# Performance work log

Measured on AMD Instinct MI355X. Metric: run time of the kernel, lower is better.

## Reference

```python
import jax, jax.numpy as jnp
import numpy as np

N = 100000
K = 27  # 3^3 kernel offsets for dimension=3
EPS = 1e-6


def layer_norm(x, gamma, beta):
    mu = jnp.mean(x, axis=-1, keepdims=True)
    var = jnp.mean(jnp.square(x - mu), axis=-1, keepdims=True)
    return (x - mu) * jax.lax.rsqrt(var + EPS) * gamma + beta


def sparse_conv3(x, idx, mask, W):
    # gather-GEMM-scatter form of Minkowski sparse conv:
    # x: [N, Cin], idx/mask: [N, K], W: [K, Cin, Cout]
    xg = jnp.where(mask[..., None], x[idx], 0.0)  # [N, K, Cin]
    return jnp.einsum('nkc,kcd->nd', xg, W)


def setup_inputs() -> dict:
    key = jax.random.key(0)
    ks = jax.random.split(key, 6)
    x = jax.random.normal(ks[0], (N, 32), dtype=jnp.float32)
    neighbor_idx = jax.random.randint(ks[1], (N, K), 0, N, dtype=jnp.int32)
    neighbor_mask = jax.random.randint(ks[2], (N, K), 0, 2) > 0
    W_conv = jax.random.normal(ks[3], (32, 32), dtype=jnp.float32) * 0.1
    W1 = jax.random.normal(ks[4], (K, 32, 128), dtype=jnp.float32) * 0.05
    W2 = jax.random.normal(ks[5], (K, 128, 32), dtype=jnp.float32) * 0.05
    return {
        'x': x,
        'neighbor_idx': neighbor_idx,
        'neighbor_mask': neighbor_mask,
        'W_conv': W_conv,
        'gamma0': jnp.ones((32,), jnp.float32),
        'beta0': jnp.zeros((32,), jnp.float32),
        'W1': W1,
        'gamma1': jnp.ones((128,), jnp.float32),
        'beta1': jnp.zeros((128,), jnp.float32),
        'W2': W2,
        'gamma2': jnp.ones((32,), jnp.float32),
        'beta2': jnp.zeros((32,), jnp.float32),
    }


def reference(x, neighbor_idx, neighbor_mask, W_conv, gamma0, beta0,
              W1, gamma1, beta1, W2, gamma2, beta2):
    gelu = lambda t: jax.nn.gelu(t, approximate=False)  # torch default (erf)
    residual = x
    out = x @ W_conv                      # kernel_size=1 conv == dense matmul
    out = gelu(layer_norm(out, gamma0, beta0))
    out = sparse_conv3(out, neighbor_idx, neighbor_mask, W1)
    out = gelu(layer_norm(out, gamma1, beta1))
    out = sparse_conv3(out, neighbor_idx, neighbor_mask, W2)
    out = layer_norm(out, gamma2, beta2)
    out = out + residual
    return gelu(out)
```

## Files before the change

kernel.cpp:

```cpp
#include <hip/hip_runtime.h>
#include <hip/hip_bf16.h>
#include <math.h>

#define NPTS 100000
#define KOFF 27

typedef __attribute__((ext_vector_type(8))) __bf16 bf16x8;
typedef __attribute__((ext_vector_type(4))) float f32x4;

__device__ __forceinline__ unsigned short f2bf(float f) {
    unsigned int u = __float_as_uint(f);
    u += 0x7fffu + ((u >> 16) & 1u);
    return (unsigned short)(u >> 16);
}

__device__ __forceinline__ float gelu_erf(float v) {
    return 0.5f * v * (1.0f + erff(v * 0.70710678118654752f));
}

__global__ __launch_bounds__(256)
void repack_kernel(const float* __restrict__ W1, const float* __restrict__ W2,
                   const void* __restrict__ maskp,
                   unsigned short* __restrict__ W1p,
                   unsigned short* __restrict__ W2p,
                   unsigned short* __restrict__ W2q,
                   int* __restrict__ flagp) {
    int o = blockIdx.x * 256 + threadIdx.x;
    if (o == 0) {
        const unsigned int* mw = (const unsigned int*)maskp;
        int f = 0;
        for (int i = 0; i < 64; ++i) f |= (mw[i] > 1u) ? 1 : 0;
        *flagp = f;
    }
    if (o < KOFF * 32 * 128) {
        int j = o & 7, lane = (o >> 3) & 63;
        int quad = lane >> 4, nn = lane & 15;
        int ct1 = (o >> 9) & 7, k1 = o >> 12;
        int kk1 = quad * 8 + j;
        W1p[o] = f2bf(W1[(k1 * 32 + kk1) * 128 + (ct1 * 16 + nn)]);
        int ct2 = (o >> 9) & 1, kc2 = (o >> 10) & 3, k2 = o >> 12;
        int kk2 = kc2 * 32 + quad * 8 + j;
        W2p[o] = f2bf(W2[(k2 * 128 + kk2) * 32 + (ct2 * 16 + nn)]);
        W2q[o] = f2bf(W2[(k2 * 128 + kk2) * 32 + (2 * nn + ct2)]);
    }
}

__global__ __launch_bounds__(256)
void conv1_ln_gelu(const float* __restrict__ x, const float* __restrict__ Wc,
                   const float* __restrict__ g0, const float* __restrict__ b0,
                   unsigned short* __restrict__ out0) {
    __shared__ float xs[256];
    __shared__ float wc[1024];
    int t = threadIdx.x;
    int nb = blockIdx.x * 8;
    xs[t] = x[nb * 32 + t];
    for (int i = t; i < 1024; i += 256) wc[i] = Wc[i];
    __syncthreads();
    int r = t >> 5, d = t & 31;
    const float* xr = &xs[r * 32];
    float v = 0.f;
#pragma unroll
    for (int c = 0; c < 32; ++c) v = fmaf(xr[c], wc[c * 32 + d], v);
    float s = v, s2 = v * v;
#pragma unroll
    for (int m = 16; m >= 1; m >>= 1) {
        s  += __shfl_xor(s,  m, 32);
        s2 += __shfl_xor(s2, m, 32);
    }
    float mu  = s * (1.f / 32.f);
    float var = s2 * (1.f / 32.f) - mu * mu;
    float y = (v - mu) * rsqrtf(var + 1e-6f) * g0[d] + b0[d];
    out0[nb * 32 + t] = f2bf(gelu_erf(y));
}

__device__ __forceinline__ void stage_gidx64(int* s_gidx, const int* nidx,
                                             const void* maskp, int mflag,
                                             int nb, int t) {
    int cnt = (NPTS - nb < 64 ? NPTS - nb : 64) * KOFF;
    for (int i = t; i < 64 * KOFF; i += 64) {
        int g = -1;
        if (i < cnt) {
            int gi = nidx[nb * KOFF + i];
            int m = mflag ? (int)((const unsigned char*)maskp)[nb * KOFF + i]
                          : ((const int*)maskp)[nb * KOFF + i];
            g = m ? gi : -1;
        }
        s_gidx[i] = g;
    }
}

__global__ __launch_bounds__(64, 2)
void conv_k1(const int* __restrict__ nidx, const void* __restrict__ maskp,
             const int* __restrict__ flagp,
             const unsigned short* __restrict__ out0,
             const unsigned short* __restrict__ W1p,
             const float* __restrict__ g1, const float* __restrict__ b1,
             unsigned short* __restrict__ out1) {
    __shared__ int s_gidx[32 * KOFF];

    int t = threadIdx.x;
    int nb = blockIdx.x * 32;
    int mflag = *flagp;
    {
        for (int i = t; i < 32 * KOFF; i += 64) {
            int gi = nidx[nb * KOFF + i];
            int m = mflag ? (int)((const unsigned char*)maskp)[nb * KOFF + i]
                          : ((const int*)maskp)[nb * KOFF + i];
            s_gidx[i] = m ? gi : -1;
        }
    }
    __syncthreads();

    int lane = t & 63;
    int mrow = lane & 15, quad = lane >> 4;
    const unsigned short* a_base = out0 + quad * 8;
    const int* gp0 = &s_gidx[(0 * 16 + mrow) * KOFF];
    const int* gp1 = &s_gidx[(1 * 16 + mrow) * KOFF];

    f32x4 acc[2][8] = {};
    bf16x8 a[3][2], b[3][8];

#pragma unroll
    for (int d = 0; d < 2; ++d) {
        const unsigned short* wb = W1p + (((d * 8) * 64 + lane) << 3);
#pragma unroll
        for (int ct = 0; ct < 8; ++ct)
            b[d][ct] = *reinterpret_cast<const bf16x8*>(wb + ((ct * 64) << 3));
        int g0 = gp0[d], g1i = gp1[d];
        a[d][0] = bf16x8{}; if (g0  >= 0) a[d][0] = *reinterpret_cast<const bf16x8*>(a_base + g0  * 32);
        a[d][1] = bf16x8{}; if (g1i >= 0) a[d][1] = *reinterpret_cast<const bf16x8*>(a_base + g1i * 32);
    }

#pragma unroll
    for (int k = 0; k < KOFF; ++k) {
        if (k + 2 < KOFF) {
            int s = (k + 2) % 3;
            const unsigned short* wb = W1p + ((((k + 2) * 8) * 64 + lane) << 3);
#pragma unroll
            for (int ct = 0; ct < 8; ++ct)
                b[s][ct] = *reinterpret_cast<const bf16x8*>(wb + ((ct * 64) << 3));
            int g0 = gp0[k + 2], g1i = gp1[k + 2];
            a[s][0] = bf16x8{}; if (g0  >= 0) a[s][0] = *reinterpret_cast<const bf16x8*>(a_base + g0  * 32);
            a[s][1] = bf16x8{}; if (g1i >= 0) a[s][1] = *reinterpret_cast<const bf16x8*>(a_base + g1i * 32);
        }
#pragma unroll
        for (int rt = 0; rt < 2; ++rt)
#pragma unroll
            for (int ct = 0; ct < 8; ++ct)
                acc[rt][ct] = __builtin_amdgcn_mfma_f32_16x16x32_bf16(a[k % 3][rt], b[k % 3][ct], acc[rt][ct], 0, 0, 0);
    }

    float gv[8], bv[8];
#pragma unroll
    for (int ct = 0; ct < 8; ++ct) {
        gv[ct] = g1[ct * 16 + mrow];
        bv[ct] = b1[ct * 16 + mrow];
    }
#pragma unroll
    for (int rt = 0; rt < 2; ++rt) {
        int n_base = nb + rt * 16 + quad * 4;
#pragma unroll
        for (int r = 0; r < 4; ++r) {
            float s = 0.f, s2 = 0.f;
#pragma unroll
            for (int ct = 0; ct < 8; ++ct) { float v = acc[rt][ct][r]; s += v; s2 += v * v; }
#pragma unroll
            for (int m = 1; m <= 8; m <<= 1) {
                s  += __shfl_xor(s,  m, 16);
                s2 += __shfl_xor(s2, m, 16);
            }
            float mu = s * (1.f / 128.f);
            float rs = rsqrtf(s2 * (1.f / 128.f) - mu * mu + 1e-6f);
            int n = n_base + r;
#pragma unroll
            for (int ct = 0; ct < 8; ++ct) {
                float y = (acc[rt][ct][r] - mu) * rs * gv[ct] + bv[ct];
                out1[n * 128 + ct * 16 + mrow] = f2bf(gelu_erf(y));
            }
        }
    }
}

__global__ __launch_bounds__(64, 2)
void gemm_tmp(const unsigned short* __restrict__ out1,
              const unsigned short* __restrict__ W2q,
              unsigned short* __restrict__ tmp) {
    int t = threadIdx.x;
    int nb = blockIdx.x * 64;
    int mrow = t & 15, quad = t >> 4;

    bf16x8 a[4][4];
#pragma unroll
    for (int rt = 0; rt < 4; ++rt) {
        int n = nb + rt * 16 + mrow;
        bool ok = (n < NPTS);
#pragma unroll
        for (int kc = 0; kc < 4; ++kc) {
            a[rt][kc] = bf16x8{};
            if (ok)
                a[rt][kc] = *reinterpret_cast<const bf16x8*>(out1 + (size_t)n * 128 + kc * 32 + quad * 8);
        }
    }
    bf16x8 b[2][8];
    {
        const unsigned short* wb = W2q + (t << 3);
#pragma unroll
        for (int f = 0; f < 8; ++f)
            b[0][f] = *reinterpret_cast<const bf16x8*>(wb + ((f * 64) << 3));
    }

#pragma unroll
    for (int k = 0; k < KOFF; ++k) {
        int cur = k & 1, nxt = cur ^ 1;
        if (k + 1 < KOFF) {
            const unsigned short* wb = W2q + ((((k + 1) * 8) * 64 + t) << 3);
#pragma unroll
            for (int f = 0; f < 8; ++f)
                b[nxt][f] = *reinterpret_cast<const bf16x8*>(wb + ((f * 64) << 3));
        }
        f32x4 acc[4][2] = {};
#pragma unroll
        for (int rt = 0; rt < 4; ++rt)
#pragma unroll
            for (int kc = 0; kc < 4; ++kc) {
                acc[rt][0] = __builtin_amdgcn_mfma_f32_16x16x32_bf16(a[rt][kc], b[cur][kc * 2 + 0], acc[rt][0], 0, 0, 0);
                acc[rt][1] = __builtin_amdgcn_mfma_f32_16x16x32_bf16(a[rt][kc], b[cur][kc * 2 + 1], acc[rt][1], 0, 0, 0);
            }
        unsigned int* tk32 = (unsigned int*)(tmp + (size_t)k * NPTS * 32);
#pragma unroll
        for (int rt = 0; rt < 4; ++rt) {
            int n0 = nb + rt * 16 + quad * 4;
#pragma unroll
            for (int r = 0; r < 4; ++r) {
                int n = n0 + r;
                if (n < NPTS) {
                    unsigned int pk = (unsigned int)f2bf(acc[rt][0][r])
                                    | ((unsigned int)f2bf(acc[rt][1][r]) << 16);
                    tk32[(size_t)n * 16 + mrow] = pk;
                }
            }
        }
    }
}

__global__ __launch_bounds__(256)
void gather_sum(const int* __restrict__ nidx, const void* __restrict__ maskp,
                const int* __restrict__ flagp,
                const unsigned short* __restrict__ tmp,
                const float* __restrict__ g2, const float* __restrict__ b2,
                const float* __restrict__ x, float* __restrict__ outp) {
    __shared__ int s_gidx[64 * KOFF];
    int t = threadIdx.x;
    int nb = blockIdx.x * 64;
    int mflag = *flagp;
    int cnt = (NPTS - nb < 64 ? NPTS - nb : 64) * KOFF;
    for (int i = t; i < 64 * KOFF; i += 256) {
        int g = -1;
        if (i < cnt) {
            int gi = nidx[nb * KOFF + i];
            int m = mflag ? (int)((const unsigned char*)maskp)[nb * KOFF + i]
                          : ((const int*)maskp)[nb * KOFF + i];
            g = m ? gi : -1;
        }
        s_gidx[i] = g;
    }
    __syncthreads();

    int rl = t >> 2, q = t & 3;
    const int* gp = &s_gidx[rl * KOFF];
    const unsigned short* tq = tmp + q * 8;

    float acc[8] = {};
    uint4 ring[4];
#pragma unroll
    for (int d = 0; d < 4; ++d) {
        int g = gp[d];
        ring[d] = uint4{0u, 0u, 0u, 0u};
        if (g >= 0)
            ring[d] = *reinterpret_cast<const uint4*>(tq + ((size_t)d * NPTS + g) * 32);
    }
#pragma unroll
    for (int k = 0; k < KOFF; ++k) {
        uint4 v = ring[k & 3];
        if (k + 4 < KOFF) {
            int g = gp[k + 4];
            ring[k & 3] = uint4{0u, 0u, 0u, 0u};
            if (g >= 0)
                ring[k & 3] = *reinterpret_cast<const uint4*>(tq + ((size_t)(k + 4) * NPTS + g) * 32);
        }
        unsigned int w0 = v.x, w1 = v.y, w2 = v.z, w3 = v.w;
        acc[0] += __uint_as_float(w0 << 16);
        acc[1] += __uint_as_float(w0 & 0xffff0000u);
        acc[2] += __uint_as_float(w1 << 16);
        acc[3] += __uint_as_float(w1 & 0xffff0000u);
        acc[4] += __uint_as_float(w2 << 16);
        acc[5] += __uint_as_float(w2 & 0xffff0000u);
        acc[6] += __uint_as_float(w3 << 16);
        acc[7] += __uint_as_float(w3 & 0xffff0000u);
    }

    float s = 0.f, s2 = 0.f;
#pragma unroll
    for (int j = 0; j < 8; ++j) { s += acc[j]; s2 += acc[j] * acc[j]; }
    s += __shfl_xor(s, 1); s2 += __shfl_xor(s2, 1);
    s += __shfl_xor(s, 2); s2 += __shfl_xor(s2, 2);
    float mu = s * (1.f / 32.f);
    float rs = rsqrtf(s2 * (1.f / 32.f) - mu * mu + 1e-6f);

    int n = nb + rl;
    if (n < NPTS) {
        float o[8];
#pragma unroll
        for (int j = 0; j < 8; ++j) {
            int c = q * 8 + j;
            float y = (acc[j] - mu) * rs * g2[c] + b2[c] + x[n * 32 + c];
            o[j] = gelu_erf(y);
        }
        *reinterpret_cast<float4*>(outp + n * 32 + q * 8)     = make_float4(o[0], o[1], o[2], o[3]);
        *reinterpret_cast<float4*>(outp + n * 32 + q * 8 + 4) = make_float4(o[4], o[5], o[6], o[7]);
    }
}

__global__ __launch_bounds__(64, 2)
void conv_k2_fb(const int* __restrict__ nidx, const void* __restrict__ maskp,
                const int* __restrict__ flagp,
                const unsigned short* __restrict__ out1,
                const unsigned short* __restrict__ W2p,
                const float* __restrict__ g2, const float* __restrict__ b2,
                const float* __restrict__ x, float* __restrict__ outp) {
    __shared__ int s_gidx[64 * KOFF];

    int t = threadIdx.x;
    int nb = blockIdx.x * 64;
    int mflag = *flagp;
    stage_gidx64(s_gidx, nidx, maskp, mflag, nb, t);
    __syncthreads();

    int lane = t & 63;
    int mrow = lane & 15, quad = lane >> 4;
    const unsigned short* a_base = out1 + quad * 8;
    const int* gp0 = &s_gidx[(0 * 16 + mrow) * KOFF];
    const int* gp1 = &s_gidx[(1 * 16 + mrow) * KOFF];
    const int* gp2 = &s_gidx[(2 * 16 + mrow) * KOFF];
    const int* gp3 = &s_gidx[(3 * 16 + mrow) * KOFF];

    f32x4 acc[4][2] = {};
    bf16x8 a[2][4][4], b[2][8];

    {
        const unsigned short* wb = W2p + (lane << 3);
#pragma unroll
        for (int f = 0; f < 8; ++f)
            b[0][f] = *reinterpret_cast<const bf16x8*>(wb + ((f * 64) << 3));
        int gg[4] = { gp0[0], gp1[0], gp2[0], gp3[0] };
#pragma unroll
        for (int rt = 0; rt < 4; ++rt) {
#pragma unroll
            for (int kc = 0; kc < 4; ++kc) a[0][rt][kc] = bf16x8{};
            if (gg[rt] >= 0) {
#pragma unroll
                for (int kc = 0; kc < 4; ++kc)
                    a[0][rt][kc] = *reinterpret_cast<const bf16x8*>(a_base + (size_t)gg[rt] * 128 + kc * 32);
            }
        }
    }

#pragma unroll
    for (int k = 0; k < KOFF; ++k) {
        int cur = k & 1, nxt = cur ^ 1;
        if (k + 1 < KOFF) {
            const unsigned short* wb = W2p + ((((k + 1) * 8) * 64 + lane) << 3);
#pragma unroll
            for (int f = 0; f < 8; ++f)
                b[nxt][f] = *reinterpret_cast<const bf16x8*>(wb + ((f * 64) << 3));
            int gg[4] = { gp0[k + 1], gp1[k + 1], gp2[k + 1], gp3[k + 1] };
#pragma unroll
            for (int rt = 0; rt < 4; ++rt) {
#pragma unroll
                for (int kc = 0; kc < 4; ++kc) a[nxt][rt][kc] = bf16x8{};
                if (gg[rt] >= 0) {
#pragma unroll
                    for (int kc = 0; kc < 4; ++kc)
                        a[nxt][rt][kc] = *reinterpret_cast<const bf16x8*>(a_base + (size_t)gg[rt] * 128 + kc * 32);
                }
            }
        }
#pragma unroll
        for (int rt = 0; rt < 4; ++rt)
#pragma unroll
            for (int kc = 0; kc < 4; ++kc) {
                acc[rt][0] = __builtin_amdgcn_mfma_f32_16x16x32_bf16(a[cur][rt][kc], b[cur][kc * 2 + 0], acc[rt][0], 0, 0, 0);
                acc[rt][1] = __builtin_amdgcn_mfma_f32_16x16x32_bf16(a[cur][rt][kc], b[cur][kc * 2 + 1], acc[rt][1], 0, 0, 0);
            }
    }

    float gv0 = g2[mrow], gv1 = g2[mrow + 16];
    float bv0 = b2[mrow], bv1 = b2[mrow + 16];
#pragma unroll
    for (int rt = 0; rt < 4; ++rt) {
        int n_base = nb + rt * 16 + quad * 4;
#pragma unroll
        for (int r = 0; r < 4; ++r) {
            float v0 = acc[rt][0][r], v1 = acc[rt][1][r];
            float s = v0 + v1, s2 = v0 * v0 + v1 * v1;
#pragma unroll
            for (int m = 1; m <= 8; m <<= 1) {
                s  += __shfl_xor(s,  m, 16);
                s2 += __shfl_xor(s2, m, 16);
            }
            float mu = s * (1.f / 32.f);
            float rs = rsqrtf(s2 * (1.f / 32.f) - mu * mu + 1e-6f);
            int n = n_base + r;
            if (n < NPTS) {
                float y0 = (v0 - mu) * rs * gv0 + bv0 + x[n * 32 + mrow];
                float y1 = (v1 - mu) * rs * gv1 + bv1 + x[n * 32 + mrow + 16];
                outp[n * 32 + mrow]      = gelu_erf(y0);
                outp[n * 32 + mrow + 16] = gelu_erf(y1);
            }
        }
    }
}

extern "C" void kernel_launch(void* const* d_in, const int* in_sizes, int n_in,
                              void* d_out, int out_size, void* d_ws, size_t ws_size,
                              hipStream_t stream) {
    const float* x    = (const float*)d_in[0];
    const int*   nidx = (const int*)d_in[1];
    const void*  maskp = d_in[2];
    const float* Wc = (const float*)d_in[3];
    const float* g0 = (const float*)d_in[4];
    const float* b0 = (const float*)d_in[5];
    const float* W1 = (const float*)d_in[6];
    const float* g1 = (const float*)d_in[7];
    const float* b1 = (const float*)d_in[8];
    const float* W2 = (const float*)d_in[9];
    const float* g2 = (const float*)d_in[10];
    const float* b2 = (const float*)d_in[11];

    char* ws = (char*)d_ws;
    unsigned short* out0 = (unsigned short*)ws;
    unsigned short* out1 = (unsigned short*)(ws + 6400000);
    unsigned short* W1p  = (unsigned short*)(ws + 32000000);
    unsigned short* W2p  = (unsigned short*)(ws + 32221184);
    unsigned short* W2q  = (unsigned short*)(ws + 32442368);
    int* flagp           = (int*)(ws + 32663552);
    unsigned short* tmp  = (unsigned short*)(ws + 32663616);
    const size_t NEED_TMP = 32663616UL + (size_t)KOFF * NPTS * 32 * 2;

    repack_kernel<<<432, 256, 0, stream>>>(W1, W2, maskp, W1p, W2p, W2q, flagp);
    conv1_ln_gelu<<<NPTS / 8, 256, 0, stream>>>(x, Wc, g0, b0, out0);
    conv_k1<<<NPTS / 32, 64, 0, stream>>>(nidx, maskp, flagp, out0, W1p, g1, b1, out1);
    if (ws_size >= NEED_TMP) {
        gemm_tmp<<<(NPTS + 63) / 64, 64, 0, stream>>>(out1, W2q, tmp);
        gather_sum<<<(NPTS + 63) / 64, 256, 0, stream>>>(nidx, maskp, flagp, tmp, g2, b2, x, (float*)d_out);
    } else {
        conv_k2_fb<<<(NPTS + 63) / 64, 64, 0, stream>>>(nidx, maskp, flagp, out1, W2p, g2, b2, x, (float*)d_out);
    }
}
```

Before: 269.7 us.

## Share W1 slices through LDS across four waves in first sparse conv

The first sparse-conv kernel now runs 256-thread blocks covering 128 points. Four waves share W1 weight slices staged in LDS, six kernel offsets per phase, instead of each 64-thread block reading the weights from global memory itself. Gather prefetch depth grows from 2 to 4 offsets. This cuts redundant global and L2 weight traffic, but adds block-wide barriers between phases, more registers and a larger LDS footprint, which may reduce occupancy.

New measurement: 287.3 us. +6.5%, slower.

```diff
diff --git a/kernel.cpp b/kernel.cpp
--- a/kernel.cpp
+++ b/kernel.cpp
@@ -89,65 +89,100 @@
     }
 }
 
-__global__ __launch_bounds__(64, 2)
+#define RPB 128
+#define PH_SL 6
+
+__global__ __launch_bounds__(256, 2)
 void conv_k1(const int* __restrict__ nidx, const void* __restrict__ maskp,
              const int* __restrict__ flagp,
              const unsigned short* __restrict__ out0,
              const unsigned short* __restrict__ W1p,
              const float* __restrict__ g1, const float* __restrict__ b1,
              unsigned short* __restrict__ out1) {
-    __shared__ int s_gidx[32 * KOFF];
+    __shared__ int s_gidx[RPB * KOFF];
+    __shared__ unsigned short b_lds[PH_SL * 4096];
 
     int t = threadIdx.x;
-    int nb = blockIdx.x * 32;
+    int nb = blockIdx.x * RPB;
     int mflag = *flagp;
+
     {
-        for (int i = t; i < 32 * KOFF; i += 64) {
-            int gi = nidx[nb * KOFF + i];
-            int m = mflag ? (int)((const unsigned char*)maskp)[nb * KOFF + i]
-                          : ((const int*)maskp)[nb * KOFF + i];
-            s_gidx[i] = m ? gi : -1;
-        }
+        int cnt = (NPTS - nb < RPB ? NPTS - nb : RPB) * KOFF;
+        for (int i = t; i < RPB * KOFF; i += 256) {
+            int g = -1;
+            if (i < cnt) {
+                int gi = nidx[nb * KOFF + i];
+                int m = mflag ? (int)((const unsigned char*)maskp)[nb * KOFF + i]
+                              : ((const int*)maskp)[nb * KOFF + i];
+                g = m ? gi : -1;
+            }
+            s_gidx[i] = g;
+        }
+    }
+    {
+        const uint4* src = (const uint4*)W1p;
+        uint4* dst = (uint4*)b_lds;
+        for (int i = t; i < PH_SL * 512; i += 256) dst[i] = src[i];
     }
     __syncthreads();
 
-    int lane = t & 63;
+    int lane = t & 63, w = t >> 6;
     int mrow = lane & 15, quad = lane >> 4;
     const unsigned short* a_base = out0 + quad * 8;
-    const int* gp0 = &s_gidx[(0 * 16 + mrow) * KOFF];
-    const int* gp1 = &s_gidx[(1 * 16 + mrow) * KOFF];
+    const int* gp0 = &s_gidx[(w * 32 + mrow) * KOFF];
+    const int* gp1 = &s_gidx[(w * 32 + 16 + mrow) * KOFF];
 
     f32x4 acc[2][8] = {};
-    bf16x8 a[3][2], b[3][8];
-
-#pragma unroll
-    for (int d = 0; d < 2; ++d) {
-        const unsigned short* wb = W1p + (((d * 8) * 64 + lane) << 3);
-#pragma unroll
-        for (int ct = 0; ct < 8; ++ct)
-            b[d][ct] = *reinterpret_cast<const bf16x8*>(wb + ((ct * 64) << 3));
+    bf16x8 a[5][2];
+    bf16x8 bf[2][8];
+
+#pragma unroll
+    for (int d = 0; d < 4; ++d) {
         int g0 = gp0[d], g1i = gp1[d];
         a[d][0] = bf16x8{}; if (g0  >= 0) a[d][0] = *reinterpret_cast<const bf16x8*>(a_base + g0  * 32);
         a[d][1] = bf16x8{}; if (g1i >= 0) a[d][1] = *reinterpret_cast<const bf16x8*>(a_base + g1i * 32);
     }
-
-#pragma unroll
-    for (int k = 0; k < KOFF; ++k) {
-        if (k + 2 < KOFF) {
-            int s = (k + 2) % 3;
-            const unsigned short* wb = W1p + ((((k + 2) * 8) * 64 + lane) << 3);
+#pragma unroll
+    for (int ct = 0; ct < 8; ++ct)
+        bf[0][ct] = *reinterpret_cast<const bf16x8*>(&b_lds[0 * 4096 + ct * 512 + lane * 8]);
+
+#pragma unroll
+    for (int p = 0; p < 5; ++p) {
+        const int kend = (p < 4) ? PH_SL : (KOFF - 4 * PH_SL);
+#pragma unroll
+        for (int kk = 0; kk < PH_SL; ++kk) {
+            if (kk >= kend) break;
+            const int k = p * PH_SL + kk;
+            if (kk + 1 < kend) {
+#pragma unroll
+                for (int ct = 0; ct < 8; ++ct)
+                    bf[(kk + 1) & 1][ct] = *reinterpret_cast<const bf16x8*>(
+                        &b_lds[(kk + 1) * 4096 + ct * 512 + lane * 8]);
+            }
+            if (k + 4 < KOFF) {
+                int s = (k + 4) % 5;
+                int g0 = gp0[k + 4], g1i = gp1[k + 4];
+                a[s][0] = bf16x8{}; if (g0  >= 0) a[s][0] = *reinterpret_cast<const bf16x8*>(a_base + g0  * 32);
+                a[s][1] = bf16x8{}; if (g1i >= 0) a[s][1] = *reinterpret_cast<const bf16x8*>(a_base + g1i * 32);
+            }
+#pragma unroll
+            for (int rt = 0; rt < 2; ++rt)
+#pragma unroll
+                for (int ct = 0; ct < 8; ++ct)
+                    acc[rt][ct] = __builtin_amdgcn_mfma_f32_16x16x32_bf16(
+                        a[k % 5][rt], bf[kk & 1][ct], acc[rt][ct], 0, 0, 0);
+        }
+        __syncthreads();
+        if (p < 4) {
+            const int nsl = (p + 1 < 4) ? PH_SL : (KOFF - 4 * PH_SL);
+            const uint4* src = (const uint4*)W1p + (p + 1) * (PH_SL * 512);
+            uint4* dst = (uint4*)b_lds;
+            for (int i = t; i < nsl * 512; i += 256) dst[i] = src[i];
+            __syncthreads();
 #pragma unroll
             for (int ct = 0; ct < 8; ++ct)
-                b[s][ct] = *reinterpret_cast<const bf16x8*>(wb + ((ct * 64) << 3));
-            int g0 = gp0[k + 2], g1i = gp1[k + 2];
-            a[s][0] = bf16x8{}; if (g0  >= 0) a[s][0] = *reinterpret_cast<const bf16x8*>(a_base + g0  * 32);
-            a[s][1] = bf16x8{}; if (g1i >= 0) a[s][1] = *reinterpret_cast<const bf16x8*>(a_base + g1i * 32);
-        }
-#pragma unroll
-        for (int rt = 0; rt < 2; ++rt)
-#pragma unroll
-            for (int ct = 0; ct < 8; ++ct)
-                acc[rt][ct] = __builtin_amdgcn_mfma_f32_16x16x32_bf16(a[k % 3][rt], b[k % 3][ct], acc[rt][ct], 0, 0, 0);
+                bf[0][ct] = *reinterpret_cast<const bf16x8*>(&b_lds[0 * 4096 + ct * 512 + lane * 8]);
+        }
     }
 
     float gv[8], bv[8];
@@ -158,7 +193,7 @@
     }
 #pragma unroll
     for (int rt = 0; rt < 2; ++rt) {
-        int n_base = nb + rt * 16 + quad * 4;
+        int n_base = nb + w * 32 + rt * 16 + quad * 4;
 #pragma unroll
         for (int r = 0; r < 4; ++r) {
             float s = 0.f, s2 = 0.f;
@@ -172,10 +207,12 @@
             float mu = s * (1.f / 128.f);
             float rs = rsqrtf(s2 * (1.f / 128.f) - mu * mu + 1e-6f);
             int n = n_base + r;
-#pragma unroll
-            for (int ct = 0; ct < 8; ++ct) {
-                float y = (acc[rt][ct][r] - mu) * rs * gv[ct] + bv[ct];
-                out1[n * 128 + ct * 16 + mrow] = f2bf(gelu_erf(y));
+            if (n < NPTS) {
+#pragma unroll
+                for (int ct = 0; ct < 8; ++ct) {
+                    float y = (acc[rt][ct][r] - mu) * rs * gv[ct] + bv[ct];
+                    out1[n * 128 + ct * 16 + mrow] = f2bf(gelu_erf(y));
+                }
             }
         }
     }
@@ -449,7 +486,7 @@
 
     repack_kernel<<<432, 256, 0, stream>>>(W1, W2, maskp, W1p, W2p, W2q, flagp);
     conv1_ln_gelu<<<NPTS / 8, 256, 0, stream>>>(x, Wc, g0, b0, out0);
-    conv_k1<<<NPTS / 32, 64, 0, stream>>>(nidx, maskp, flagp, out0, W1p, g1, b1, out1);
+    conv_k1<<<(NPTS + RPB - 1) / RPB, 256, 0, stream>>>(nidx, maskp, flagp, out0, W1p, g1, b1, out1);
     if (ws_size >= NEED_TMP) {
         gemm_tmp<<<(NPTS + 63) / 64, 64, 0, stream>>>(out1, W2q, tmp);
         gather_sum<<<(NPTS + 63) / 64, 256, 0, stream>>>(nidx, maskp, flagp, tmp, g2, b2, x, (float*)d_out);
```
